# Optimization experiments

Hardware: AMD Instinct MI355X
Metric: run time of the kernel (lower is better)

The kernel has to match this reference:

```python
import jax, jax.numpy as jnp
import numpy as np

N_NODES = 50000
N_EDGES = 800000
NODE_IN = 16
NODE_OUT = 3
H = 128
N_LAYERS = 3


def setup_inputs() -> dict:
    key = jax.random.key(0)
    ks = jax.random.split(key, 16)
    s = 0.05
    inp = {
        "x": jax.random.normal(ks[0], (N_NODES, NODE_IN), dtype=jnp.float32),
        "edge_index": jax.random.randint(ks[1], (2, N_EDGES), 0, N_NODES, dtype=jnp.int64),
        # encoder / decoder
        "enc_w": jax.random.normal(ks[2], (NODE_IN, H), dtype=jnp.float32) * s,
        "enc_b": jnp.zeros((H,), dtype=jnp.float32),
        "dec_w": jax.random.normal(ks[3], (H, NODE_OUT), dtype=jnp.float32) * s,
        "dec_b": jnp.zeros((NODE_OUT,), dtype=jnp.float32),
        # 3 processor layers, edge MLP: Linear(2H,H) -> ReLU -> Linear(H,H)
        "edge_w1": jax.random.normal(ks[4], (N_LAYERS, 2 * H, H), dtype=jnp.float32) * s,
        "edge_b1": jnp.zeros((N_LAYERS, H), dtype=jnp.float32),
        "edge_w2": jax.random.normal(ks[5], (N_LAYERS, H, H), dtype=jnp.float32) * s,
        "edge_b2": jnp.zeros((N_LAYERS, H), dtype=jnp.float32),
        # node MLP: Linear(2H,H) -> ReLU -> Linear(H,H)
        "node_w1": jax.random.normal(ks[6], (N_LAYERS, 2 * H, H), dtype=jnp.float32) * s,
        "node_b1": jnp.zeros((N_LAYERS, H), dtype=jnp.float32),
        "node_w2": jax.random.normal(ks[7], (N_LAYERS, H, H), dtype=jnp.float32) * s,
        "node_b2": jnp.zeros((N_LAYERS, H), dtype=jnp.float32),
    }
    return inp


def reference(x, edge_index, enc_w, enc_b, dec_w, dec_b,
              edge_w1, edge_b1, edge_w2, edge_b2,
              node_w1, node_b1, node_w2, node_b2):
    row = edge_index[0]  # source nodes
    col = edge_index[1]  # destination nodes
    h = x @ enc_w + enc_b  # [N, H]
    for l in range(N_LAYERS):
        # EdgeModel: cat(src, dest) -> MLP
        e_in = jnp.concatenate([h[row], h[col]], axis=1)  # [E, 2H]
        e = jnp.maximum(e_in @ edge_w1[l] + edge_b1[l], 0.0) @ edge_w2[l] + edge_b2[l]  # [E, H]
        # NodeModel: scatter_add messages by col, cat with x -> MLP
        agg = jax.ops.segment_sum(e, col, num_segments=h.shape[0])  # [N, H]
        n_in = jnp.concatenate([h, agg], axis=1)  # [N, 2H]
        h_upd = jnp.maximum(n_in @ node_w1[l] + node_b1[l], 0.0) @ node_w2[l] + node_b2[l]
        h = h + h_upd  # residual
    return h @ dec_w + dec_b  # [N, NODE_OUT]
```

## Files before the change

kernel.cpp:

```cpp
#include <hip/hip_runtime.h>
#include <hip/hip_bf16.h>
#include <stdint.h>

#define N_NODES 50000
#define N_EDGES 800000
#define HID 128
#define NODE_IN 16
#define NODE_OUT 3
#define EDGE_TILES 12500
#define NODE_TILES 782
#define SCAN_BLOCKS 196
#define EDGE_BLOCKS 3125
#define MFOLD_BLOCKS 192

typedef __attribute__((ext_vector_type(8))) short short8;
typedef __attribute__((ext_vector_type(4))) float f32x4;
typedef __attribute__((ext_vector_type(4))) unsigned int u32x4;

__device__ __forceinline__ unsigned short f2bf(float f) {
    union { float f; unsigned int u; } v; v.f = f;
    unsigned int u = v.u;
    u += 0x7fff + ((u >> 16) & 1);
    return (unsigned short)(u >> 16);
}
__device__ __forceinline__ float bf2f(unsigned short s) {
    union { unsigned int u; float f; } v; v.u = ((unsigned int)s) << 16;
    return v.f;
}
__device__ __forceinline__ float bfu_lo(unsigned int u) {
    union { unsigned int u; float f; } v; v.u = u << 16; return v.f;
}
__device__ __forceinline__ float bfu_hi(unsigned int u) {
    union { unsigned int u; float f; } v; v.u = u & 0xffff0000u; return v.f;
}
__device__ __forceinline__ unsigned int cvt_pk_bf16(float lo, float hi) {
    unsigned int r;
    asm("v_cvt_pk_bf16_f32 %0, %1, %2" : "=v"(r) : "v"(lo), "v"(hi));
    return r;
}

__global__ __launch_bounds__(256) void k1_hist_mfold(
    const int* __restrict__ colp, int* __restrict__ cnt, int* __restrict__ rank,
    const float* __restrict__ edge_w2, const float* __restrict__ node_w1,
    const float* __restrict__ edge_b2,
    float* __restrict__ Mtmp, float* __restrict__ Vtmp) {
    int b = blockIdx.x, t = threadIdx.x;
    if (b < EDGE_BLOCKS) {
        int e = b * 256 + t;
        rank[e] = atomicAdd(&cnt[colp[e]], 1);
    } else {
        int d = (b - EDGE_BLOCKS) * 256 + t;
        int L = d / 16384, rem = d & 16383;
        int k = rem >> 7, n = rem & 127;
        const float* w2  = edge_w2 + (size_t)L * 16384;
        const float* w1b = node_w1 + (size_t)L * 32768 + 16384;
        float acc = 0.f;
        #pragma unroll 4
        for (int j = 0; j < 128; j++) acc += w2[k * 128 + j] * w1b[j * 128 + n];
        Mtmp[d] = acc;
        if (k == 0) {
            const float* b2 = edge_b2 + (size_t)L * 128;
            float vv = 0.f;
            #pragma unroll 4
            for (int j = 0; j < 128; j++) vv += b2[j] * w1b[j * 128 + n];
            Vtmp[L * 128 + n] = vv;
        }
    }
}

__global__ __launch_bounds__(256) void k2a_scan1_swizzle(
    const int* __restrict__ cnt, int* __restrict__ ex, int* __restrict__ bsums,
    const float* __restrict__ edge_w1, const float* __restrict__ node_w1,
    const float* __restrict__ node_w2, const float* __restrict__ Mtmp,
    unsigned short* __restrict__ swz) {
    __shared__ int s[256];
    int b = blockIdx.x, t = threadIdx.x;
    if (b < SCAN_BLOCKS) {
        int i = b * 256 + t;
        int v = (i < N_NODES) ? cnt[i] : 0;
        s[t] = v;
        __syncthreads();
        for (int off = 1; off < 256; off <<= 1) {
            int u = (t >= off) ? s[t - off] : 0;
            __syncthreads();
            s[t] += u;
            __syncthreads();
        }
        if (i < N_NODES) ex[i] = s[t] - v;
        if (t == 255) bsums[b] = s[255];
    } else {
        for (int d = (b - SCAN_BLOCKS) * 256 + t; d < 3 * 98304;
             d += (gridDim.x - SCAN_BLOCKS) * 256) {
            int L = d / 98304;
            int rem = d - L * 98304;
            unsigned short* base = swz + L * 98304;
            if (rem < 32768) {
                const float* w1 = edge_w1 + (size_t)L * 32768;
                int j = rem & 7, ll = (rem >> 3) & 63, tt = rem >> 9;
                int nt = tt & 15, kt = tt >> 4;
                int k = kt * 32 + ((ll >> 4) << 3) + j;
                int cc = nt * 16 + (ll & 15);
                float v = (cc < 128) ? w1[k * 128 + cc] : w1[(128 + k) * 128 + (cc - 128)];
                base[rem] = f2bf(v);
            } else if (rem < 49152) {
            } else if (rem < 81920) {
                int d2 = rem - 49152;
                int j = d2 & 7, ll = (d2 >> 3) & 63, tt = d2 >> 9;
                int nt = tt & 7, kt = tt >> 3;
                int k = kt * 32 + ((ll >> 4) << 3) + j, n = (nt << 4) + (ll & 15);
                float v = (k < 128) ? node_w1[(size_t)L * 32768 + k * 128 + n]
                                    : Mtmp[(size_t)L * 16384 + (k - 128) * 128 + n];
                base[rem] = f2bf(v);
            } else {
                int d2 = rem - 81920;
                const float* src = node_w2 + (size_t)L * 16384;
                int j = d2 & 7, ll = (d2 >> 3) & 63, tt = d2 >> 9;
                int nt = tt & 7, kt = tt >> 3;
                int k = kt * 32 + ((ll >> 4) << 3) + j, n = (nt << 4) + (ll & 15);
                base[rem] = f2bf(src[k * 128 + n]);
            }
        }
    }
}

__global__ __launch_bounds__(256) void k3a_scatter(
    const int* __restrict__ rowp, const int* __restrict__ colp,
    const int* __restrict__ ex, const int* __restrict__ bsums,
    const int* __restrict__ rank, int2* __restrict__ rc_sorted) {
    __shared__ int sc[256];
    __shared__ int ls[SCAN_BLOCKS];
    int t = threadIdx.x;
    int v = (t < SCAN_BLOCKS) ? bsums[t] : 0;
    sc[t] = v;
    __syncthreads();
    for (int off = 1; off < 256; off <<= 1) {
        int u = (t >= off) ? sc[t - off] : 0;
        __syncthreads();
        sc[t] += u;
        __syncthreads();
    }
    if (t < SCAN_BLOCKS) ls[t] = sc[t] - v;
    __syncthreads();

    int e = blockIdx.x * 256 + t;
    if (e >= N_EDGES) return;
    int c = colp[e];
    int pos = ex[c] + ls[c >> 8] + rank[e];
    rc_sorted[pos] = make_int2(rowp[e], c);
}

__global__ __launch_bounds__(256, 4) void k3b_encoder_sd(
    const float* __restrict__ x, const float* __restrict__ enc_w, const float* __restrict__ enc_b,
    const unsigned short* __restrict__ w1c, const float* __restrict__ eb1,
    unsigned short* __restrict__ h,
    unsigned short* __restrict__ S, unsigned short* __restrict__ D, float* __restrict__ aggH)
{
    __shared__ float wts[NODE_IN * HID];
    __shared__ float bts[HID];
    __shared__ float xs[64][NODE_IN];
    __shared__ unsigned short hs[64][136];
    int t = threadIdx.x, wave = t >> 6, l = t & 63, q = l >> 4, l16 = l & 15;
    int n0 = blockIdx.x * 64;
    int nt0s = wave * 4;

    for (int i = t; i < NODE_IN * HID; i += 256) wts[i] = enc_w[i];
    if (t < HID) bts[t] = enc_b[t];
    for (int i = t; i < 64 * NODE_IN; i += 256) {
        int nl = i >> 4, ii = i & 15;
        int n = n0 + nl;
        xs[nl][ii] = (n < N_NODES) ? x[n * NODE_IN + ii] : 0.f;
    }
    for (int o = t; o < 64 * 32; o += 256) {
        int nl = o >> 5, c4 = o & 31;
        int n = n0 + nl;
        if (n < N_NODES) *(f32x4*)&aggH[n * HID + c4 * 4] = (f32x4){0.f, 0.f, 0.f, 0.f};
    }
    short8 wr[4][4];
    #pragma unroll
    for (int kt = 0; kt < 4; kt++)
        #pragma unroll
        for (int i = 0; i < 4; i++)
            wr[kt][i] = *(const short8*)(w1c + ((kt * 16 + nt0s + i) * 64 + l) * 8);
    __syncthreads();

    for (int o = t; o < 64 * HID; o += 256) {
        int nl = o >> 7, cc = o & 127;
        float acc = bts[cc];
        #pragma unroll
        for (int i = 0; i < NODE_IN; i++) acc += xs[nl][i] * wts[i * HID + cc];
        unsigned short hb = f2bf(acc);
        hs[nl][cc] = hb;
        int n = n0 + nl;
        if (n < N_NODES) h[n * HID + cc] = hb;
    }
    __syncthreads();

    f32x4 acc[4][4];
    #pragma unroll
    for (int g = 0; g < 4; g++)
        #pragma unroll
        for (int i = 0; i < 4; i++) acc[g][i] = (f32x4){0.f, 0.f, 0.f, 0.f};
    #pragma unroll
    for (int kt = 0; kt < 4; kt++) {
        #pragma unroll
        for (int g = 0; g < 4; g++) {
            short8 a = *(const short8*)&hs[g * 16 + l16][kt * 32 + q * 8];
            #pragma unroll
            for (int i = 0; i < 4; i++)
                acc[g][i] = __builtin_amdgcn_mfma_f32_16x16x32_bf16(a, wr[kt][i], acc[g][i], 0, 0, 0);
        }
    }
    #pragma unroll
    for (int i = 0; i < 4; i++) {
        int cc = (nt0s + i) * 16 + l16;
        float badd = 0.f;
        if (cc >= 128) badd = eb1[cc - 128];
        #pragma unroll
        for (int g = 0; g < 4; g++)
            #pragma unroll
            for (int r = 0; r < 4; r++) {
                int n = n0 + g * 16 + q * 4 + r;
                if (n < N_NODES) {
                    unsigned short v = f2bf(acc[g][i][r] + badd);
                    if (cc < 128) S[n * HID + cc] = v;
                    else          D[n * HID + (cc - 128)] = v;
                }
            }
    }
}

__global__ __launch_bounds__(256, 8) void edge_kernel(
    const unsigned short* __restrict__ S, const unsigned short* __restrict__ D,
    const int2* __restrict__ rc_sorted, float* __restrict__ aggH)
{
    __shared__ unsigned short hid_s[64][136];
    __shared__ int row_s[64], col_s[64];
    int t = threadIdx.x;
    int l = t & 63, w = t >> 6;
    int ch = l & 15, eg = l >> 4;
    int rbase = w * 16;
    int c128 = t & 127, r0 = (t >> 7) * 32;

    const int TPX = (EDGE_TILES + 7) / 8;
    int xcd = blockIdx.x & 7, slot = blockIdx.x >> 3;

    for (int i = slot; i < TPX; i += 256) {
        int tile = xcd * TPX + i;
        if (tile >= EDGE_TILES) break;
        int e0 = tile * 64 + rbase;
        if (l < 16) {
            int2 rc = rc_sorted[e0 + l];
            row_s[rbase + l] = rc.x;
            col_s[rbase + l] = rc.y;
        }
        asm volatile("s_waitcnt lgkmcnt(0)" ::: "memory");
        __builtin_amdgcn_sched_barrier(0);

        #pragma unroll
        for (int it = 0; it < 4; it++) {
            int el = rbase + it * 4 + eg;
            int r = row_s[el], c = col_s[el];
            short8 sv = *(const short8*)(S + (size_t)r * HID + ch * 8);
            short8 dv = *(const short8*)(D + (size_t)c * HID + ch * 8);
            u32x4 o;
            #pragma unroll
            for (int p = 0; p < 4; p++) {
                unsigned int us = ((const unsigned int*)&sv)[p];
                unsigned int ud = ((const unsigned int*)&dv)[p];
                float v0 = bfu_lo(us) + bfu_lo(ud);
                float v1 = bfu_hi(us) + bfu_hi(ud);
                v0 = v0 > 0.f ? v0 : 0.f;
                v1 = v1 > 0.f ? v1 : 0.f;
                o[p] = cvt_pk_bf16(v0, v1);
            }
            *(u32x4*)&hid_s[el][ch * 8] = o;
        }
        __syncthreads();

        float acc = 0.f;
        int cur = col_s[r0];
        #pragma unroll
        for (int i0 = 0; i0 < 32; i0 += 4) {
            int4 c4 = *(const int4*)&col_s[r0 + i0];
            #pragma unroll
            for (int j = 0; j < 4; j++) {
                int c = ((const int*)&c4)[j];
                if (c != cur) {
                    unsafeAtomicAdd(&aggH[(size_t)cur * HID + c128], acc);
                    acc = 0.f;
                    cur = c;
                }
                acc += bf2f(hid_s[r0 + i0 + j][c128]);
            }
        }
        unsafeAtomicAdd(&aggH[(size_t)cur * HID + c128], acc);
        __syncthreads();
    }
}

template<int LAST>
__global__ __launch_bounds__(256, 4) void node_kernel(
    unsigned short* __restrict__ h, float* __restrict__ aggH, const int* __restrict__ cnt,
    const unsigned short* __restrict__ w1m_s, const float* __restrict__ b1,
    const float* __restrict__ vfold,
    const unsigned short* __restrict__ w2s, const float* __restrict__ b2,
    const unsigned short* __restrict__ w1c_next, const float* __restrict__ eb1n,
    unsigned short* __restrict__ S, unsigned short* __restrict__ D,
    const float* __restrict__ dec_w, const float* __restrict__ dec_b, float* __restrict__ out)
{
    __shared__ unsigned short in_h[64][136];
    __shared__ unsigned short in_a[64][136];
    __shared__ int cnt_s[64];
    __shared__ float dw[HID * NODE_OUT];
    __shared__ float db[NODE_OUT];
    int t = threadIdx.x, wave = t >> 6, l = t & 63, q = l >> 4, l16 = l & 15;
    int nt0 = wave * 2, nt0s = wave * 4;
    int n0 = blockIdx.x * 64;

    if (LAST) {
        for (int i = t; i < HID * NODE_OUT; i += 256) dw[i] = dec_w[i];
        if (t < NODE_OUT) db[t] = dec_b[t];
    }

    #pragma unroll
    for (int it = 0; it < 8; it++) {
        int g = it * 256 + t;
        int nl = g >> 5, sub = g & 31, half = sub >> 4, li = sub & 15;
        int n = n0 + nl;
        short8 v = (short8){0, 0, 0, 0, 0, 0, 0, 0};
        if (n < N_NODES) {
            if (half == 0) {
                v = *(const short8*)(h + n * HID + li * 8);
            } else {
                float* ap = aggH + n * HID + li * 8;
                f32x4 a0 = *(f32x4*)ap, a1 = *(f32x4*)(ap + 4);
                unsigned int* vp = (unsigned int*)&v;
                vp[0] = cvt_pk_bf16(a0[0], a0[1]);
                vp[1] = cvt_pk_bf16(a0[2], a0[3]);
                vp[2] = cvt_pk_bf16(a1[0], a1[1]);
                vp[3] = cvt_pk_bf16(a1[2], a1[3]);
                if (!LAST) {
                    *(f32x4*)ap       = (f32x4){0.f, 0.f, 0.f, 0.f};
                    *(f32x4*)(ap + 4) = (f32x4){0.f, 0.f, 0.f, 0.f};
                }
            }
        }
        if (half == 0) *(short8*)&in_h[nl][li * 8] = v;
        else           *(short8*)&in_a[nl][li * 8] = v;
    }
    if (t < 64) cnt_s[t] = (n0 + t < N_NODES) ? cnt[n0 + t] : 0;
    __syncthreads();

    float b1r0 = b1[nt0 * 16 + l16], b1r1 = b1[(nt0 + 1) * 16 + l16];
    float vr0 = vfold[nt0 * 16 + l16], vr1 = vfold[(nt0 + 1) * 16 + l16];
    float b2r0 = b2[nt0 * 16 + l16], b2r1 = b2[(nt0 + 1) * 16 + l16];

    f32x4 acc[4][2];
    #pragma unroll
    for (int g = 0; g < 4; g++)
        #pragma unroll
        for (int j = 0; j < 2; j++) acc[g][j] = (f32x4){0.f, 0.f, 0.f, 0.f};
    #pragma unroll
    for (int kt = 0; kt < 8; kt++) {
        short8 b0 = *(const short8*)(w1m_s + ((kt * 8 + nt0)     * 64 + l) * 8);
        short8 b1v = *(const short8*)(w1m_s + ((kt * 8 + nt0 + 1) * 64 + l) * 8);
        #pragma unroll
        for (int g = 0; g < 4; g++) {
            short8 a = (kt < 4) ? *(const short8*)&in_h[g * 16 + l16][kt * 32 + q * 8]
                                : *(const short8*)&in_a[g * 16 + l16][(kt - 4) * 32 + q * 8];
            acc[g][0] = __builtin_amdgcn_mfma_f32_16x16x32_bf16(a, b0, acc[g][0], 0, 0, 0);
            acc[g][1] = __builtin_amdgcn_mfma_f32_16x16x32_bf16(a, b1v, acc[g][1], 0, 0, 0);
        }
    }
    __syncthreads();

    #pragma unroll
    for (int j = 0; j < 2; j++) {
        float bv = j ? b1r1 : b1r0;
        float vv = j ? vr1 : vr0;
        #pragma unroll
        for (int g = 0; g < 4; g++)
            #pragma unroll
            for (int r = 0; r < 4; r++) {
                int m2 = g * 16 + q * 4 + r;
                float v = acc[g][j][r] + bv + (float)cnt_s[m2] * vv;
                v = v > 0.f ? v : 0.f;
                in_a[m2][(nt0 + j) * 16 + l16] = f2bf(v);
            }
    }
    __syncthreads();

    f32x4 acc2[4][2];
    #pragma unroll
    for (int g = 0; g < 4; g++)
        #pragma unroll
        for (int j = 0; j < 2; j++) acc2[g][j] = (f32x4){0.f, 0.f, 0.f, 0.f};
    #pragma unroll
    for (int kt = 0; kt < 4; kt++) {
        short8 b0 = *(const short8*)(w2s + ((kt * 8 + nt0)     * 64 + l) * 8);
        short8 b1v = *(const short8*)(w2s + ((kt * 8 + nt0 + 1) * 64 + l) * 8);
        #pragma unroll
        for (int g = 0; g < 4; g++) {
            short8 a = *(const short8*)&in_a[g * 16 + l16][kt * 32 + q * 8];
            acc2[g][0] = __builtin_amdgcn_mfma_f32_16x16x32_bf16(a, b0, acc2[g][0], 0, 0, 0);
            acc2[g][1] = __builtin_amdgcn_mfma_f32_16x16x32_bf16(a, b1v, acc2[g][1], 0, 0, 0);
        }
    }
    #pragma unroll
    for (int j = 0; j < 2; j++) {
        float bv = j ? b2r1 : b2r0;
        #pragma unroll
        for (int g = 0; g < 4; g++)
            #pragma unroll
            for (int r = 0; r < 4; r++) {
                float v = acc2[g][j][r] + bv;
                int m2 = g * 16 + q * 4 + r;
                int n = n0 + m2;
                if (n < N_NODES) {
                    int c = (nt0 + j) * 16 + l16;
                    unsigned short nh = f2bf(bf2f(in_h[m2][c]) + v);
                    if (!LAST) h[n * HID + c] = nh;
                    in_h[m2][c] = nh;
                }
            }
    }
    __syncthreads();

    if (!LAST) {
        #pragma unroll
        for (int p = 0; p < 2; p++) {
            short8 wr[4][2];
            #pragma unroll
            for (int kt = 0; kt < 4; kt++) {
                wr[kt][0] = *(const short8*)(w1c_next + ((kt * 16 + nt0s + p * 2)     * 64 + l) * 8);
                wr[kt][1] = *(const short8*)(w1c_next + ((kt * 16 + nt0s + p * 2 + 1) * 64 + l) * 8);
            }
            f32x4 accs[4][2];
            #pragma unroll
            for (int g = 0; g < 4; g++)
                #pragma unroll
                for (int i = 0; i < 2; i++) accs[g][i] = (f32x4){0.f, 0.f, 0.f, 0.f};
            #pragma unroll
            for (int kt = 0; kt < 4; kt++) {
                #pragma unroll
                for (int g = 0; g < 4; g++) {
                    short8 a = *(const short8*)&in_h[g * 16 + l16][kt * 32 + q * 8];
                    accs[g][0] = __builtin_amdgcn_mfma_f32_16x16x32_bf16(a, wr[kt][0], accs[g][0], 0, 0, 0);
                    accs[g][1] = __builtin_amdgcn_mfma_f32_16x16x32_bf16(a, wr[kt][1], accs[g][1], 0, 0, 0);
                }
            }
            #pragma unroll
            for (int i = 0; i < 2; i++) {
                int c = (nt0s + p * 2 + i) * 16 + l16;
                float badd = 0.f;
                if (c >= 128) badd = eb1n[c - 128];
                #pragma unroll
                for (int g = 0; g < 4; g++)
                    #pragma unroll
                    for (int r = 0; r < 4; r++) {
                        int n = n0 + g * 16 + q * 4 + r;
                        if (n < N_NODES) {
                            unsigned short v = f2bf(accs[g][i][r] + badd);
                            if (c < 128) S[n * HID + c] = v;
                            else         D[n * HID + (c - 128)] = v;
                        }
                    }
            }
        }
    } else {
        if (t < 64 * NODE_OUT) {
            int nl = t / 3, o = t - 3 * nl;
            int n = n0 + nl;
            if (n < N_NODES) {
                float a = db[o];
                #pragma unroll 4
                for (int k = 0; k < HID; k++) a += bf2f(in_h[nl][k]) * dw[k * 3 + o];
                out[n * 3 + o] = a;
            }
        }
    }
}

extern "C" void kernel_launch(void* const* d_in, const int* in_sizes, int n_in,
                              void* d_out, int out_size, void* d_ws, size_t ws_size,
                              hipStream_t stream) {
    const float* x       = (const float*)d_in[0];
    const int*   ei      = (const int*)d_in[1];
    const float* enc_w   = (const float*)d_in[2];
    const float* enc_b   = (const float*)d_in[3];
    const float* dec_w   = (const float*)d_in[4];
    const float* dec_b   = (const float*)d_in[5];
    const float* edge_w1 = (const float*)d_in[6];
    const float* edge_b1 = (const float*)d_in[7];
    const float* edge_w2 = (const float*)d_in[8];
    const float* edge_b2 = (const float*)d_in[9];
    const float* node_w1 = (const float*)d_in[10];
    const float* node_b1 = (const float*)d_in[11];
    const float* node_w2 = (const float*)d_in[12];
    const float* node_b2 = (const float*)d_in[13];

    char* ws = (char*)d_ws;
    unsigned short* h    = (unsigned short*)ws;
    float*          aggH = (float*)(ws + 12800000);
    unsigned short* swz  = (unsigned short*)(ws + 38400000);
    int* cnt             = (int*)(ws + 38989824);
    int* ex              = (int*)(ws + 39189824);
    int* bsums           = (int*)(ws + 39389824);
    int2* rc_sorted      = (int2*)(ws + 39390848);
    unsigned short* Sbuf = (unsigned short*)(ws + 45790848);
    unsigned short* Dbuf = (unsigned short*)(ws + 58590848);
    float* Mtmp          = (float*)(ws + 71390848);
    float* Vtmp          = (float*)(ws + 71587456);
    int* rank            = (int*)(ws + 58590848);

    const int* rowp = ei;
    const int* colp = ei + N_EDGES;

    hipMemsetAsync(cnt, 0, (size_t)N_NODES * 4, stream);

    k1_hist_mfold<<<EDGE_BLOCKS + MFOLD_BLOCKS, 256, 0, stream>>>(
        colp, cnt, rank, edge_w2, node_w1, edge_b2, Mtmp, Vtmp);
    k2a_scan1_swizzle<<<SCAN_BLOCKS + 288, 256, 0, stream>>>(cnt, ex, bsums, edge_w1,
                                                             node_w1, node_w2, Mtmp, swz);
    k3a_scatter<<<3125, 256, 0, stream>>>(rowp, colp, ex, bsums, rank, rc_sorted);
    k3b_encoder_sd<<<NODE_TILES, 256, 0, stream>>>(x, enc_w, enc_b, swz ,
                                                   edge_b1 , h,
                                                   Sbuf, Dbuf, aggH);

    for (int L = 0; L < 3; L++) {
        unsigned short* base = swz + (size_t)L * 98304;
        unsigned short* next = swz + (size_t)(L + 1) * 98304;
        edge_kernel<<<2048, 256, 0, stream>>>(Sbuf, Dbuf, rc_sorted, aggH);
        if (L < 2) {
            node_kernel<0><<<NODE_TILES, 256, 0, stream>>>(
                h, aggH, cnt,
                base + 49152, node_b1 + (size_t)L * HID, Vtmp + (size_t)L * HID,
                base + 81920, node_b2 + (size_t)L * HID,
                next, edge_b1 + (size_t)(L + 1) * HID, Sbuf, Dbuf, dec_w, dec_b, (float*)d_out);
        } else {
            node_kernel<1><<<NODE_TILES, 256, 0, stream>>>(
                h, aggH, cnt,
                base + 49152, node_b1 + (size_t)L * HID, Vtmp + (size_t)L * HID,
                base + 81920, node_b2 + (size_t)L * HID,
                base , edge_b1 , Sbuf, Dbuf, dec_w, dec_b, (float*)d_out);
        }
    }
}
```

Before: 385.8 us.

## Partition edge kernel by destination-node ranges with shared-memory aggregation

Each edge block now owns a contiguous range of 32 destination nodes, found through a precomputed global CSR offset array (ex2), and processes all of that range's sorted edges. Partial sums are accumulated in LDS with local atomics and written to aggH once with plain stores, replacing global float atomics. This also removes the separate zeroing of aggH in the encoder and node kernels. In exchange it adds load imbalance when node degrees vary, extra LDS use, and lower occupancy (launch bound 4 instead of 8).

```diff
diff --git a/kernel.cpp b/kernel.cpp
--- a/kernel.cpp
+++ b/kernel.cpp
@@ -7,11 +7,12 @@
 #define HID 128
 #define NODE_IN 16
 #define NODE_OUT 3
-#define EDGE_TILES 12500
 #define NODE_TILES 782
 #define SCAN_BLOCKS 196
 #define EDGE_BLOCKS 3125
 #define MFOLD_BLOCKS 192
+#define DG 32
+#define DBLOCKS 1563
 
 typedef __attribute__((ext_vector_type(8))) short short8;
 typedef __attribute__((ext_vector_type(4))) float f32x4;
@@ -126,7 +127,8 @@
 __global__ __launch_bounds__(256) void k3a_scatter(
     const int* __restrict__ rowp, const int* __restrict__ colp,
     const int* __restrict__ ex, const int* __restrict__ bsums,
-    const int* __restrict__ rank, int2* __restrict__ rc_sorted) {
+    const int* __restrict__ rank, int2* __restrict__ rc_sorted,
+    int* __restrict__ ex2) {
     __shared__ int sc[256];
     __shared__ int ls[SCAN_BLOCKS];
     int t = threadIdx.x;
@@ -142,7 +144,13 @@
     if (t < SCAN_BLOCKS) ls[t] = sc[t] - v;
     __syncthreads();
 
-    int e = blockIdx.x * 256 + t;
+    int b = blockIdx.x;
+    if (b < SCAN_BLOCKS) {
+        int i = b * 256 + t;
+        if (i < N_NODES) ex2[i] = ex[i] + ls[b];
+    }
+
+    int e = b * 256 + t;
     if (e >= N_EDGES) return;
     int c = colp[e];
     int pos = ex[c] + ls[c >> 8] + rank[e];
@@ -153,7 +161,7 @@
     const float* __restrict__ x, const float* __restrict__ enc_w, const float* __restrict__ enc_b,
     const unsigned short* __restrict__ w1c, const float* __restrict__ eb1,
     unsigned short* __restrict__ h,
-    unsigned short* __restrict__ S, unsigned short* __restrict__ D, float* __restrict__ aggH)
+    unsigned short* __restrict__ S, unsigned short* __restrict__ D)
 {
     __shared__ float wts[NODE_IN * HID];
     __shared__ float bts[HID];
@@ -170,11 +178,6 @@
         int n = n0 + nl;
         xs[nl][ii] = (n < N_NODES) ? x[n * NODE_IN + ii] : 0.f;
     }
-    for (int o = t; o < 64 * 32; o += 256) {
-        int nl = o >> 5, c4 = o & 31;
-        int n = n0 + nl;
-        if (n < N_NODES) *(f32x4*)&aggH[n * HID + c4 * 4] = (f32x4){0.f, 0.f, 0.f, 0.f};
-    }
     short8 wr[4][4];
     #pragma unroll
     for (int kt = 0; kt < 4; kt++)
@@ -229,27 +232,40 @@
     }
 }
 
-__global__ __launch_bounds__(256, 8) void edge_kernel(
+__global__ __launch_bounds__(256, 4) void edge_kernel(
     const unsigned short* __restrict__ S, const unsigned short* __restrict__ D,
-    const int2* __restrict__ rc_sorted, float* __restrict__ aggH)
+    const int2* __restrict__ rc_sorted, const int* __restrict__ ex2,
+    float* __restrict__ aggH)
 {
     __shared__ unsigned short hid_s[64][136];
     __shared__ int row_s[64], col_s[64];
+    __shared__ float aggL[DG][HID];
     int t = threadIdx.x;
     int l = t & 63, w = t >> 6;
     int ch = l & 15, eg = l >> 4;
     int rbase = w * 16;
     int c128 = t & 127, r0 = (t >> 7) * 32;
 
-    const int TPX = (EDGE_TILES + 7) / 8;
+    const int q = DBLOCKS / 8, r = DBLOCKS % 8;
     int xcd = blockIdx.x & 7, slot = blockIdx.x >> 3;
-
-    for (int i = slot; i < TPX; i += 256) {
-        int tile = xcd * TPX + i;
-        if (tile >= EDGE_TILES) break;
-        int e0 = tile * 64 + rbase;
+    int cntx = q + (xcd < r);
+    if (slot >= cntx) return;
+    int myb = xcd * q + (xcd < r ? xcd : r) + slot;
+
+    int d0 = myb * DG;
+    int d1 = d0 + DG; if (d1 > N_NODES) d1 = N_NODES;
+    int eStart = ex2[d0];
+    int eEnd = (d1 < N_NODES) ? ex2[d1] : N_EDGES;
+
+    #pragma unroll
+    for (int o = t; o < DG * HID; o += 256) aggL[o >> 7][o & 127] = 0.f;
+
+    int nst = (eEnd - eStart + 63) >> 6;
+    for (int s = 0; s < nst; s++) {
+        int es0 = eStart + s * 64;
         if (l < 16) {
-            int2 rc = rc_sorted[e0 + l];
+            int e = es0 + rbase + l;
+            int2 rc = (e < eEnd) ? rc_sorted[e] : make_int2(0, d0);
             row_s[rbase + l] = rc.x;
             col_s[rbase + l] = rc.y;
         }
@@ -259,19 +275,21 @@
         #pragma unroll
         for (int it = 0; it < 4; it++) {
             int el = rbase + it * 4 + eg;
-            int r = row_s[el], c = col_s[el];
-            short8 sv = *(const short8*)(S + (size_t)r * HID + ch * 8);
-            short8 dv = *(const short8*)(D + (size_t)c * HID + ch * 8);
-            u32x4 o;
-            #pragma unroll
-            for (int p = 0; p < 4; p++) {
-                unsigned int us = ((const unsigned int*)&sv)[p];
-                unsigned int ud = ((const unsigned int*)&dv)[p];
-                float v0 = bfu_lo(us) + bfu_lo(ud);
-                float v1 = bfu_hi(us) + bfu_hi(ud);
-                v0 = v0 > 0.f ? v0 : 0.f;
-                v1 = v1 > 0.f ? v1 : 0.f;
-                o[p] = cvt_pk_bf16(v0, v1);
+            u32x4 o = (u32x4){0u, 0u, 0u, 0u};
+            if (es0 + el < eEnd) {
+                int rr = row_s[el], c = col_s[el];
+                short8 sv = *(const short8*)(S + (size_t)rr * HID + ch * 8);
+                short8 dv = *(const short8*)(D + (size_t)c * HID + ch * 8);
+                #pragma unroll
+                for (int p = 0; p < 4; p++) {
+                    unsigned int us = ((const unsigned int*)&sv)[p];
+                    unsigned int ud = ((const unsigned int*)&dv)[p];
+                    float v0 = bfu_lo(us) + bfu_lo(ud);
+                    float v1 = bfu_hi(us) + bfu_hi(ud);
+                    v0 = v0 > 0.f ? v0 : 0.f;
+                    v1 = v1 > 0.f ? v1 : 0.f;
+                    o[p] = cvt_pk_bf16(v0, v1);
+                }
             }
             *(u32x4*)&hid_s[el][ch * 8] = o;
         }
@@ -286,15 +304,21 @@
             for (int j = 0; j < 4; j++) {
                 int c = ((const int*)&c4)[j];
                 if (c != cur) {
-                    unsafeAtomicAdd(&aggH[(size_t)cur * HID + c128], acc);
+                    atomicAdd(&aggL[cur - d0][c128], acc);
                     acc = 0.f;
                     cur = c;
                 }
                 acc += bf2f(hid_s[r0 + i0 + j][c128]);
             }
         }
-        unsafeAtomicAdd(&aggH[(size_t)cur * HID + c128], acc);
+        atomicAdd(&aggL[cur - d0][c128], acc);
         __syncthreads();
+    }
+
+    #pragma unroll
+    for (int o = t; o < DG * HID; o += 256) {
+        int d = d0 + (o >> 7);
+        if (d < d1) aggH[(size_t)d * HID + (o & 127)] = aggL[o >> 7][o & 127];
     }
 }
 
@@ -332,17 +356,13 @@
             if (half == 0) {
                 v = *(const short8*)(h + n * HID + li * 8);
             } else {
-                float* ap = aggH + n * HID + li * 8;
-                f32x4 a0 = *(f32x4*)ap, a1 = *(f32x4*)(ap + 4);
+                const float* ap = aggH + n * HID + li * 8;
+                f32x4 a0 = *(const f32x4*)ap, a1 = *(const f32x4*)(ap + 4);
                 unsigned int* vp = (unsigned int*)&v;
                 vp[0] = cvt_pk_bf16(a0[0], a0[1]);
                 vp[1] = cvt_pk_bf16(a0[2], a0[3]);
                 vp[2] = cvt_pk_bf16(a1[0], a1[1]);
                 vp[3] = cvt_pk_bf16(a1[2], a1[3]);
-                if (!LAST) {
-                    *(f32x4*)ap       = (f32x4){0.f, 0.f, 0.f, 0.f};
-                    *(f32x4*)(ap + 4) = (f32x4){0.f, 0.f, 0.f, 0.f};
-                }
             }
         }
         if (half == 0) *(short8*)&in_h[nl][li * 8] = v;
@@ -511,6 +531,7 @@
     unsigned short* Dbuf = (unsigned short*)(ws + 58590848);
     float* Mtmp          = (float*)(ws + 71390848);
     float* Vtmp          = (float*)(ws + 71587456);
+    int* ex2             = (int*)(ws + 71588992);
     int* rank            = (int*)(ws + 58590848);
 
     const int* rowp = ei;
@@ -522,15 +543,15 @@
         colp, cnt, rank, edge_w2, node_w1, edge_b2, Mtmp, Vtmp);
     k2a_scan1_swizzle<<<SCAN_BLOCKS + 288, 256, 0, stream>>>(cnt, ex, bsums, edge_w1,
                                                              node_w1, node_w2, Mtmp, swz);
-    k3a_scatter<<<3125, 256, 0, stream>>>(rowp, colp, ex, bsums, rank, rc_sorted);
+    k3a_scatter<<<3125, 256, 0, stream>>>(rowp, colp, ex, bsums, rank, rc_sorted, ex2);
     k3b_encoder_sd<<<NODE_TILES, 256, 0, stream>>>(x, enc_w, enc_b, swz ,
                                                    edge_b1 , h,
-                                                   Sbuf, Dbuf, aggH);
+                                                   Sbuf, Dbuf);
 
     for (int L = 0; L < 3; L++) {
         unsigned short* base = swz + (size_t)L * 98304;
         unsigned short* next = swz + (size_t)(L + 1) * 98304;
-        edge_kernel<<<2048, 256, 0, stream>>>(Sbuf, Dbuf, rc_sorted, aggH);
+        edge_kernel<<<1568, 256, 0, stream>>>(Sbuf, Dbuf, rc_sorted, ex2, aggH);
         if (L < 2) {
             node_kernel<0><<<NODE_TILES, 256, 0, stream>>>(
                 h, aggH, cnt,
```

Result: slower. 618.8 us (+60.4%).
